# Kernel optimization log

Hardware: AMD Instinct MI355X
Metric: run time of the kernel (lower is better)

## Reference

```python
import jax, jax.numpy as jnp
from jax import lax
import numpy as np

B, T, D_IN, H, D_L1_IN = 128, 2048, 5, 128, 256


def _gru_layer(x, w_ih, w_hh, b_ih, b_hh, reverse):
    # x: [B,T,D]; w_ih: [3H,D]; w_hh: [3H,H]. PyTorch gate order: r, z, n.
    gx = jnp.einsum('btd,gd->btg', x, w_ih) + b_ih  # [B,T,3H] input projections, batched
    if reverse:
        gx = gx[:, ::-1]
    gx_t = jnp.swapaxes(gx, 0, 1)  # [T,B,3H]
    h0 = jnp.zeros((x.shape[0], H), x.dtype)

    def step(h, gxt):
        gh = h @ w_hh.T + b_hh  # [B,3H]
        r = jax.nn.sigmoid(gxt[:, :H] + gh[:, :H])
        z = jax.nn.sigmoid(gxt[:, H:2 * H] + gh[:, H:2 * H])
        n = jnp.tanh(gxt[:, 2 * H:] + r * gh[:, 2 * H:])
        h_new = (1.0 - z) * n + z * h
        return h_new, h_new

    _, ys = lax.scan(step, h0, gx_t)  # ys: [T,B,H]
    ys = jnp.swapaxes(ys, 0, 1)  # [B,T,H]
    if reverse:
        ys = ys[:, ::-1]
    return ys


def setup_inputs() -> dict:
    key = jax.random.key(0)
    ks = jax.random.split(key, 16)
    s0 = 1.0 / np.sqrt(H)

    def w(k, shape):
        return jax.random.uniform(k, shape, jnp.float32, -s0, s0)

    inp = {'seq': jax.random.normal(ks[0], (B, T, D_IN), jnp.float32)}
    # layer 0 forward / backward (input dim 5)
    inp['w_ih_l0f'] = w(ks[1], (3 * H, D_IN)); inp['w_hh_l0f'] = w(ks[2], (3 * H, H))
    inp['b_ih_l0f'] = w(ks[3], (3 * H,));      inp['b_hh_l0f'] = w(ks[4], (3 * H,))
    inp['w_ih_l0b'] = w(ks[5], (3 * H, D_IN)); inp['w_hh_l0b'] = w(ks[6], (3 * H, H))
    inp['b_ih_l0b'] = w(ks[7], (3 * H,));      inp['b_hh_l0b'] = w(ks[8], (3 * H,))
    # layer 1 forward / backward (input dim 256 = 2*H)
    inp['w_ih_l1f'] = w(ks[9], (3 * H, D_L1_IN));  inp['w_hh_l1f'] = w(ks[10], (3 * H, H))
    inp['b_ih_l1f'] = w(ks[11], (3 * H,));         inp['b_hh_l1f'] = w(ks[12], (3 * H,))
    inp['w_ih_l1b'] = w(ks[13], (3 * H, D_L1_IN)); inp['w_hh_l1b'] = w(ks[14], (3 * H, H))
    inp['b_ih_l1b'] = w(ks[15], (3 * H,));         inp['b_hh_l1b'] = w(ks[15], (3 * H,)) * 0.9
    # linear head
    kf = jax.random.split(ks[0], 2)
    inp['fc_w'] = w(kf[0], (1, 2 * H))
    inp['fc_b'] = w(kf[1], (1,))
    return inp


def reference(seq, w_ih_l0f, w_hh_l0f, b_ih_l0f, b_hh_l0f,
              w_ih_l0b, w_hh_l0b, b_ih_l0b, b_hh_l0b,
              w_ih_l1f, w_hh_l1f, b_ih_l1f, b_hh_l1f,
              w_ih_l1b, w_hh_l1b, b_ih_l1b, b_hh_l1b,
              fc_w, fc_b):
    # layer 0: bidirectional, concat directions
    y0f = _gru_layer(seq, w_ih_l0f, w_hh_l0f, b_ih_l0f, b_hh_l0f, reverse=False)
    y0b = _gru_layer(seq, w_ih_l0b, w_hh_l0b, b_ih_l0b, b_hh_l0b, reverse=True)
    y0 = jnp.concatenate([y0f, y0b], axis=-1)  # [B,T,256]
    # layer 1
    y1f = _gru_layer(y0, w_ih_l1f, w_hh_l1f, b_ih_l1f, b_hh_l1f, reverse=False)
    y1b = _gru_layer(y0, w_ih_l1b, w_hh_l1b, b_ih_l1b, b_hh_l1b, reverse=True)
    y1 = jnp.concatenate([y1f, y1b], axis=-1)  # [B,T,256]
    # head on last timestep
    return y1[:, -1, :] @ fc_w.T + fc_b  # [B,1]
```

## Files before the change

### kernel.cpp

```cpp
#include <hip/hip_runtime.h>
#include <hip/hip_fp16.h>
#include <cstdint>

#define B_   128
#define T_   2048
#define DIN  5
#define H_   128
#define G3   384
#define D1   256
#define CH   128
#define NCH  (T_ / CH)
#define LOG2CH 7

typedef _Float16 half8 __attribute__((ext_vector_type(8)));
typedef float f32x4 __attribute__((ext_vector_type(4)));

__device__ __forceinline__ float sigmoid_f(float x) {
    return __builtin_amdgcn_rcpf(1.0f + __expf(-x));
}
__device__ __forceinline__ float tanh_f(float x) {
    return 1.0f - 2.0f * __builtin_amdgcn_rcpf(__expf(2.0f * x) + 1.0f);
}
__device__ __forceinline__ unsigned long long pack4h(const float* h) {
    union { __half2 h2[2]; unsigned long long u; } pk;
    pk.h2[0] = __floats2half2_rn(h[0], h[1]);
    pk.h2[1] = __floats2half2_rn(h[2], h[3]);
    return pk.u;
}
__device__ __forceinline__ f32x4 h4_to_f(unsigned long long u) {
    union { unsigned long long u; __half2 h2[2]; } p; p.u = u;
    const float2 a = __half22float2(p.h2[0]);
    const float2 b = __half22float2(p.h2[1]);
    f32x4 r; r[0] = a.x; r[1] = a.y; r[2] = b.x; r[3] = b.y; return r;
}
__device__ __forceinline__ void fast_barrier() {
    asm volatile("s_waitcnt lgkmcnt(0)\n\ts_barrier" ::: "memory");
}

__global__ __launch_bounds__(512, 2) void scan0_mfma4(
    const float* __restrict__ seq,
    const float* __restrict__ wihf, const float* __restrict__ whhf,
    const float* __restrict__ bihf, const float* __restrict__ bhhf,
    const float* __restrict__ wihb, const float* __restrict__ whhb,
    const float* __restrict__ bihb, const float* __restrict__ bhhb,
    __half* __restrict__ y0)
{
    const int tid = threadIdx.x;
    const int w  = tid >> 6;
    const int l  = tid & 63;
    const int lo = l & 15;
    const int g  = l >> 4;
    const int dir = blockIdx.x >> 3;
    const int bg  = blockIdx.x & 7;

    const float* w_ih = dir ? wihb : wihf;
    const float* w_hh = dir ? whhb : whhf;
    const float* b_ih = dir ? bihb : bihf;
    const float* b_hh = dir ? bhhb : bhhf;

    __shared__ __align__(16) char smem[2 * 16 * 512];

    half8 a_r[5], a_z[5], a_n[5], a_x;
    {
        const int grow = w * 16 + lo;
#pragma unroll
        for (int c = 0; c < 5; ++c) {
            half8 vr, vz, vn;
#pragma unroll
            for (int j = 0; j < 8; ++j) {
                const int k = c * 32 + g * 8 + j;
                float fr, fz, fn;
                if (k < 128) {
                    fr = w_hh[grow * H_ + k];
                    fz = w_hh[(128 + grow) * H_ + k];
                    fn = w_hh[(256 + grow) * H_ + k];
                } else if (k < 133) {
                    fr = w_ih[grow * DIN + (k - 128)];
                    fz = w_ih[(128 + grow) * DIN + (k - 128)];
                    fn = 0.f;
                } else if (k == 133) {
                    fr = b_ih[grow] + b_hh[grow];
                    fz = b_ih[128 + grow] + b_hh[128 + grow];
                    fn = b_hh[256 + grow];
                } else { fr = 0.f; fz = 0.f; fn = 0.f; }
                vr[j] = (_Float16)fr; vz[j] = (_Float16)fz; vn[j] = (_Float16)fn;
            }
            a_r[c] = vr; a_z[c] = vz; a_n[c] = vn;
        }
        half8 vx;
#pragma unroll
        for (int j = 0; j < 8; ++j) {
            const int k = 128 + g * 8 + j;
            float f = 0.f;
            if (k < 133)       f = w_ih[(256 + grow) * DIN + (k - 128)];
            else if (k == 133) f = b_ih[256 + grow];
            vx[j] = (_Float16)f;
        }
        a_x = vx;
    }

#pragma unroll
    for (int q = 0; q < 2; ++q) {
        f32x4 z = {0.f, 0.f, 0.f, 0.f};
        *reinterpret_cast<f32x4*>(smem + tid * 32 + q * 16) = z;
    }
    __syncthreads();
    if (tid < 32) {
        const int row = tid & 15, bu = tid >> 4;
        *(_Float16*)(smem + bu * 8192 + row * 512 + (266 ^ ((row & 7) << 4))) =
            (_Float16)1.0f;
    }
    const bool stager = tid < 80;
    const int sb = tid / 5, sd = tid % 5;
    const size_t seqbase = (size_t)(bg * 16 + sb) * T_ * DIN + sd;
    float x_t1 = 0.f;
    if (stager) {
        const int tt0 = dir ? (T_ - 1) : 0;
        const float x0 = seq[seqbase + (size_t)tt0 * DIN];
        *(_Float16*)(smem + sb * 512 + ((256 + 2 * sd) ^ ((sb & 7) << 4))) =
            (_Float16)x0;
        const int tt1 = dir ? (T_ - 2) : 1;
        x_t1 = seq[seqbase + (size_t)tt1 * DIN];
    }
    __syncthreads();

    float h_old[4];
#pragma unroll
    for (int q = 0; q < 4; ++q) h_old[q] = 0.f;

    for (int t = 0; t < T_; ++t) {
        char* cur = smem + (t & 1) * 8192;
        char* nxt = smem + ((t + 1) & 1) * 8192;

        if (stager)
            *(_Float16*)(nxt + sb * 512 + ((256 + 2 * sd) ^ ((sb & 7) << 4))) =
                (_Float16)x_t1;

        half8 bf[5];
#pragma unroll
        for (int c = 0; c < 5; ++c)
            bf[c] = *reinterpret_cast<const half8*>(
                cur + lo * 512 + ((c * 64 + g * 16) ^ ((lo & 7) << 4)));

        float x_t2 = 0.f;
        if (stager) {
            const int t2 = (t + 2 < T_) ? t + 2 : T_ - 1;
            const int tt2 = dir ? (T_ - 1 - t2) : t2;
            x_t2 = seq[seqbase + (size_t)tt2 * DIN];
        }

        f32x4 zr = {0.f, 0.f, 0.f, 0.f};
        f32x4 accr = zr, accz = zr, accn = zr, accx;
#pragma unroll
        for (int c = 0; c < 5; ++c) {
            accr = __builtin_amdgcn_mfma_f32_16x16x32_f16(a_r[c], bf[c], accr, 0, 0, 0);
            accz = __builtin_amdgcn_mfma_f32_16x16x32_f16(a_z[c], bf[c], accz, 0, 0, 0);
            accn = __builtin_amdgcn_mfma_f32_16x16x32_f16(a_n[c], bf[c], accn, 0, 0, 0);
        }
        accx = __builtin_amdgcn_mfma_f32_16x16x32_f16(a_x, bf[4], zr, 0, 0, 0);

        const int tt = dir ? (T_ - 1 - t) : t;
        {
            float hn[4];
#pragma unroll
            for (int q = 0; q < 4; ++q) {
                const float r = sigmoid_f(accr[q]);
                const float z = sigmoid_f(accz[q]);
                const float n = tanh_f(accx[q] + r * accn[q]);
                hn[q] = n + z * (h_old[q] - n);
                h_old[q] = hn[q];
            }
            const int j0 = w * 16 + g * 4;
            const unsigned long long pu = pack4h(hn);
            *reinterpret_cast<unsigned long long*>(
                &y0[((size_t)(bg * 16 + lo) * T_ + tt) * D1 + dir * H_ + j0]) = pu;
            *reinterpret_cast<unsigned long long*>(
                nxt + lo * 512 + ((2 * j0) ^ ((lo & 7) << 4))) = pu;
        }
        x_t1 = x_t2;
        fast_barrier();
    }
}

__device__ __forceinline__ void scan1_role(
    char* smem,
    const __half* __restrict__ gxc,
    const float* __restrict__ whh, const float* __restrict__ bhh,
    float* __restrict__ h1, int c)
{
    __builtin_amdgcn_s_setprio(1);

    const int tid = threadIdx.x;
    const int w = tid >> 6, l = tid & 63;
    const int lo = l & 15, g = l >> 4;
    const int grp = blockIdx.x;

    half8 a_r[2][4], a_z[2][4], a_n[2][4];
    float br[2][4], bz[2][4], bn[2][4];
#pragma unroll
    for (int i = 0; i < 2; ++i) {
        const int grow = (2 * w + i) * 16 + lo;
#pragma unroll
        for (int cc = 0; cc < 4; ++cc) {
            half8 vr, vz, vn;
#pragma unroll
            for (int j = 0; j < 8; ++j) {
                const int k = cc * 32 + g * 8 + j;
                vr[j] = (_Float16)whh[grow * H_ + k];
                vz[j] = (_Float16)whh[(128 + grow) * H_ + k];
                vn[j] = (_Float16)whh[(256 + grow) * H_ + k];
            }
            a_r[i][cc] = vr; a_z[i][cc] = vz; a_n[i][cc] = vn;
        }
#pragma unroll
        for (int q = 0; q < 4; ++q) {
            const int gq = (2 * w + i) * 16 + g * 4 + q;
            br[i][q] = bhh[gq];
            bz[i][q] = bhh[128 + gq];
            bn[i][q] = bhh[256 + gq];
        }
    }

#pragma unroll
    for (int q = 0; q < 2; ++q) {
        f32x4 z = {0.f, 0.f, 0.f, 0.f};
        *reinterpret_cast<f32x4*>(smem + tid * 32 + q * 16) = z;
    }
    __syncthreads();

    float h_old[2][4];
    if (c == 0) {
#pragma unroll
        for (int i = 0; i < 2; ++i)
#pragma unroll
            for (int q = 0; q < 4; ++q) h_old[i][q] = 0.f;
    } else {
#pragma unroll
        for (int i = 0; i < 2; ++i) {
            const int j0 = (2 * w + i) * 16 + g * 4;
            const f32x4 hv = *reinterpret_cast<const f32x4*>(
                &h1[(grp * 16 + lo) * H_ + j0]);
            float hn[4];
#pragma unroll
            for (int q = 0; q < 4; ++q) { h_old[i][q] = hv[q]; hn[q] = hv[q]; }
            *reinterpret_cast<unsigned long long*>(
                smem + lo * 256 + ((2 * j0) ^ ((lo & 7) << 4))) = pack4h(hn);
        }
    }
    __syncthreads();

    const __half* gxl = gxc + (size_t)(grp * 16 + lo) * CH * G3;
    unsigned long long gxc_cur[6], gxc_nxt[6];
#pragma unroll
    for (int i = 0; i < 2; ++i) {
        const int gr0 = (2 * w + i) * 16 + g * 4;
        gxc_cur[i]     = *reinterpret_cast<const unsigned long long*>(gxl + gr0);
        gxc_cur[2 + i] = *reinterpret_cast<const unsigned long long*>(gxl + 128 + gr0);
        gxc_cur[4 + i] = *reinterpret_cast<const unsigned long long*>(gxl + 256 + gr0);
    }

    for (int t = 0; t < CH; ++t) {
        char* curb = smem + (t & 1) * 4096;
        char* nxtb = smem + ((t + 1) & 1) * 4096;

        half8 bf[4];
#pragma unroll
        for (int cc = 0; cc < 4; ++cc)
            bf[cc] = *reinterpret_cast<const half8*>(
                curb + lo * 256 + ((cc * 64 + g * 16) ^ ((lo & 7) << 4)));

        const int tn = (t + 1 < CH) ? t + 1 : t;
        const __half* p = gxl + (size_t)tn * G3;
#pragma unroll
        for (int i = 0; i < 2; ++i) {
            const int gr0 = (2 * w + i) * 16 + g * 4;
            gxc_nxt[i]     = *reinterpret_cast<const unsigned long long*>(p + gr0);
            gxc_nxt[2 + i] = *reinterpret_cast<const unsigned long long*>(p + 128 + gr0);
            gxc_nxt[4 + i] = *reinterpret_cast<const unsigned long long*>(p + 256 + gr0);
        }

        f32x4 accr[2], accz[2], accn[2];
#pragma unroll
        for (int i = 0; i < 2; ++i) {
            f32x4 zr = {0.f, 0.f, 0.f, 0.f};
            accr[i] = zr; accz[i] = zr; accn[i] = zr;
#pragma unroll
            for (int cc = 0; cc < 4; ++cc) {
                accr[i] = __builtin_amdgcn_mfma_f32_16x16x32_f16(a_r[i][cc], bf[cc], accr[i], 0, 0, 0);
                accz[i] = __builtin_amdgcn_mfma_f32_16x16x32_f16(a_z[i][cc], bf[cc], accz[i], 0, 0, 0);
                accn[i] = __builtin_amdgcn_mfma_f32_16x16x32_f16(a_n[i][cc], bf[cc], accn[i], 0, 0, 0);
            }
        }

#pragma unroll
        for (int i = 0; i < 2; ++i) {
            const f32x4 gr = h4_to_f(gxc_cur[i]);
            const f32x4 gz = h4_to_f(gxc_cur[2 + i]);
            const f32x4 gn = h4_to_f(gxc_cur[4 + i]);
            float hn[4];
#pragma unroll
            for (int q = 0; q < 4; ++q) {
                const float r = sigmoid_f(accr[i][q] + br[i][q] + gr[q]);
                const float z = sigmoid_f(accz[i][q] + bz[i][q] + gz[q]);
                const float n = tanh_f(gn[q] + r * (accn[i][q] + bn[i][q]));
                hn[q] = n + z * (h_old[i][q] - n);
                h_old[i][q] = hn[q];
            }
            const int j0 = (2 * w + i) * 16 + g * 4;
            *reinterpret_cast<unsigned long long*>(
                nxtb + lo * 256 + ((2 * j0) ^ ((lo & 7) << 4))) = pack4h(hn);
        }
#pragma unroll
        for (int i = 0; i < 6; ++i) gxc_cur[i] = gxc_nxt[i];
        fast_barrier();
    }

#pragma unroll
    for (int i = 0; i < 2; ++i) {
        const int j0 = (2 * w + i) * 16 + g * 4;
        f32x4 hv;
#pragma unroll
        for (int q = 0; q < 4; ++q) hv[q] = h_old[i][q];
        *reinterpret_cast<f32x4*>(&h1[(grp * 16 + lo) * H_ + j0]) = hv;
    }
    __builtin_amdgcn_s_setprio(0);
}

__device__ __forceinline__ void gemm_role(
    char* smem, int rb,
    const __half* __restrict__ A, const float* __restrict__ W,
    const float* __restrict__ bias, __half* __restrict__ C, int c0)
{
    _Float16 (*As)[32] = reinterpret_cast<_Float16(*)[32]>(smem);
    _Float16 (*Bs)[32] = reinterpret_cast<_Float16(*)[32]>(smem + 8192);
    const int tid = threadIdx.x;
    const int wave = tid >> 6, l = tid & 63;
    const int wm = wave >> 1, wn = wave & 1;
    const int lo = l & 15, g = l >> 4;
    const int m0 = (rb & 127) * 128, n0 = (rb >> 7) * 64;

    f32x4 acc[4][2];
#pragma unroll
    for (int mt = 0; mt < 4; ++mt)
#pragma unroll
        for (int nt = 0; nt < 2; ++nt) {
            f32x4 z = {0.f, 0.f, 0.f, 0.f};
            acc[mt][nt] = z;
        }

    for (int kc = 0; kc < 256; kc += 32) {
#pragma unroll
        for (int r2 = 0; r2 < 2; ++r2) {
            const int idx = tid + r2 * 256;
            const int row = idx >> 2, seg = idx & 3;
            const int m = m0 + row, bb = m >> LOG2CH, tlq = m & (CH - 1);
            const __half* src = A + ((size_t)bb * T_ + c0 + tlq) * D1 + kc + seg * 8;
            *reinterpret_cast<uint4*>(&As[row][seg * 8]) =
                *reinterpret_cast<const uint4*>(src);
        }
        {
            const int row = tid >> 2, seg = tid & 3;
            const float* srcw = W + (size_t)(n0 + row) * D1 + kc + seg * 8;
            const float4 u0 = *reinterpret_cast<const float4*>(srcw);
            const float4 u1 = *reinterpret_cast<const float4*>(srcw + 4);
            half8 hv;
            hv[0] = (_Float16)u0.x; hv[1] = (_Float16)u0.y;
            hv[2] = (_Float16)u0.z; hv[3] = (_Float16)u0.w;
            hv[4] = (_Float16)u1.x; hv[5] = (_Float16)u1.y;
            hv[6] = (_Float16)u1.z; hv[7] = (_Float16)u1.w;
            *reinterpret_cast<half8*>(&Bs[row][seg * 8]) = hv;
        }
        __syncthreads();
        half8 af[4], bfr[2];
#pragma unroll
        for (int mt = 0; mt < 4; ++mt)
            af[mt] = *reinterpret_cast<half8*>(&As[wm * 64 + mt * 16 + lo][g * 8]);
#pragma unroll
        for (int nt = 0; nt < 2; ++nt)
            bfr[nt] = *reinterpret_cast<half8*>(&Bs[wn * 32 + nt * 16 + lo][g * 8]);
#pragma unroll
        for (int mt = 0; mt < 4; ++mt)
#pragma unroll
            for (int nt = 0; nt < 2; ++nt)
                acc[mt][nt] = __builtin_amdgcn_mfma_f32_16x16x32_f16(
                    af[mt], bfr[nt], acc[mt][nt], 0, 0, 0);
        __syncthreads();
    }
#pragma unroll
    for (int nt = 0; nt < 2; ++nt) {
        const int n = n0 + wn * 32 + nt * 16 + lo;
        const float bv = bias[n];
#pragma unroll
        for (int mt = 0; mt < 4; ++mt) {
            const int mrow = m0 + wm * 64 + mt * 16 + g * 4;
#pragma unroll
            for (int q = 0; q < 4; ++q)
                C[(size_t)(mrow + q) * G3 + n] = __float2half(acc[mt][nt][q] + bv);
        }
    }
}

__global__ __launch_bounds__(256, 1) void fused_l1(
    const __half* __restrict__ y0,
    const float* __restrict__ W1f, const float* __restrict__ b1f,
    __half* __restrict__ gbufA, __half* __restrict__ gbufB,
    const float* __restrict__ whh, const float* __restrict__ bhh,
    float* __restrict__ h1, int ci_scan, int ci_gemm)
{
    __shared__ __align__(16) char smem[12288];
    if (blockIdx.x < 8) {
        if (ci_scan >= 0) {
            const __half* gxc = (ci_scan & 1) ? gbufB : gbufA;
            scan1_role(smem, gxc, whh, bhh, h1, ci_scan);
        }
    } else {
        if (ci_gemm < NCH) {
            __half* gxc = (ci_gemm & 1) ? gbufB : gbufA;
            gemm_role(smem, (int)blockIdx.x - 8, y0, W1f, b1f, gxc, ci_gemm * CH);
        }
    }
}

__global__ __launch_bounds__(384, 1) void back1_fc(
    const __half* __restrict__ y0, const float* __restrict__ h1,
    const float* __restrict__ w_ih_1b, const float* __restrict__ b_ih_1b,
    const float* __restrict__ b_hh_1b,
    const float* __restrict__ fc_w, const float* __restrict__ fc_b,
    float* __restrict__ out)
{
    const int g = threadIdx.x;
    const int b = blockIdx.x;
    __shared__ float ylast[D1];
    __shared__ float pre_rz[2 * H_];
    __shared__ float gxn[H_], ghn[H_];
    __shared__ float hb[H_];
    __shared__ float red[H_];

    if (g < D1) ylast[g] = __half2float(y0[((size_t)b * T_ + (T_ - 1)) * D1 + g]);
    __syncthreads();

    float accb = b_ih_1b[g];
    const float* wrow = w_ih_1b + (size_t)g * D1;
#pragma unroll 8
    for (int k = 0; k < D1; k += 4) {
        const float4 v = *reinterpret_cast<const float4*>(&ylast[k]);
        const float4 wv = *reinterpret_cast<const float4*>(&wrow[k]);
        accb += v.x * wv.x + v.y * wv.y + v.z * wv.z + v.w * wv.w;
    }
    const float bh2 = b_hh_1b[g];
    if (g < 2 * H_) pre_rz[g] = accb + bh2;
    else            { gxn[g - 2 * H_] = accb; ghn[g - 2 * H_] = bh2; }
    __syncthreads();
    if (g < H_) {
        const float r = sigmoid_f(pre_rz[g]);
        const float z = sigmoid_f(pre_rz[g + H_]);
        const float n = tanh_f(gxn[g] + r * ghn[g]);
        hb[g] = (1.0f - z) * n;
    }
    __syncthreads();
    if (g < H_) red[g] = h1[b * H_ + g] * fc_w[g] + hb[g] * fc_w[H_ + g];
    __syncthreads();
    if (g == 0) {
        float s = fc_b[0];
#pragma unroll 8
        for (int k = 0; k < H_; ++k) s += red[k];
        out[b] = s;
    }
}

extern "C" void kernel_launch(void* const* d_in, const int* in_sizes, int n_in,
                              void* d_out, int out_size, void* d_ws, size_t ws_size,
                              hipStream_t stream)
{
    const float* seq      = (const float*)d_in[0];
    const float* w_ih_l0f = (const float*)d_in[1];
    const float* w_hh_l0f = (const float*)d_in[2];
    const float* b_ih_l0f = (const float*)d_in[3];
    const float* b_hh_l0f = (const float*)d_in[4];
    const float* w_ih_l0b = (const float*)d_in[5];
    const float* w_hh_l0b = (const float*)d_in[6];
    const float* b_ih_l0b = (const float*)d_in[7];
    const float* b_hh_l0b = (const float*)d_in[8];
    const float* w_ih_l1f = (const float*)d_in[9];
    const float* w_hh_l1f = (const float*)d_in[10];
    const float* b_ih_l1f = (const float*)d_in[11];
    const float* b_hh_l1f = (const float*)d_in[12];
    const float* w_ih_l1b = (const float*)d_in[13];
    const float* b_ih_l1b = (const float*)d_in[15];
    const float* b_hh_l1b = (const float*)d_in[16];
    const float* fc_w     = (const float*)d_in[17];
    const float* fc_b     = (const float*)d_in[18];
    float* out = (float*)d_out;

    const size_t y0_bytes = (size_t)B_ * T_ * D1 * sizeof(__half);
    const size_t gx_bytes = (size_t)B_ * CH * G3 * sizeof(__half);
    __half* y0h   = (__half*)d_ws;
    __half* gbufA = (__half*)((char*)d_ws + y0_bytes);
    __half* gbufB = (__half*)((char*)d_ws + y0_bytes + gx_bytes);
    float*  h1    = (float*)((char*)d_ws + y0_bytes + 2 * gx_bytes);

    hipLaunchKernelGGL(scan0_mfma4, dim3(16), dim3(512), 0, stream,
        seq, w_ih_l0f, w_hh_l0f, b_ih_l0f, b_hh_l0f,
             w_ih_l0b, w_hh_l0b, b_ih_l0b, b_hh_l0b, y0h);

    for (int i = 0; i <= NCH; ++i) {
        hipLaunchKernelGGL(fused_l1, dim3(8 + 768), dim3(256), 0, stream,
            y0h, w_ih_l1f, b_ih_l1f, gbufA, gbufB,
            w_hh_l1f, b_hh_l1f, h1, i - 1, i);
    }

    hipLaunchKernelGGL(back1_fc, dim3(B_), dim3(384), 0, stream,
        y0h, h1, w_ih_l1b, b_ih_l1b, b_hh_l1b, fc_w, fc_b, out);
}
```

Baseline: 3.437 ms.

## Use larger layer-1 time chunks and persistent GEMM blocks to cut launches

Layer-1 time chunks are now 256 steps instead of 128 when the workspace is large enough, which halves the number of fused scan+GEMM launches and the grid barriers between them. The GEMM side no longer launches one block per tile. It uses a fixed 248 blocks that grid-stride over the tiles, so together with the 8 scan blocks the grid fits on the device at once. This trades launch and chunk-boundary overhead for a longer pipeline fill and drain, a larger intermediate buffer, and more GEMM work per block that must finish alongside the sequential scan.

```diff
diff --git a/kernel.cpp b/kernel.cpp
--- a/kernel.cpp
+++ b/kernel.cpp
@@ -8,9 +8,7 @@
 #define H_   128
 #define G3   384
 #define D1   256
-#define CH   128
-#define NCH  (T_ / CH)
-#define LOG2CH 7
+#define NGB  248
 
 typedef _Float16 half8 __attribute__((ext_vector_type(8)));
 typedef float f32x4 __attribute__((ext_vector_type(4)));
@@ -186,7 +184,7 @@
     char* smem,
     const __half* __restrict__ gxc,
     const float* __restrict__ whh, const float* __restrict__ bhh,
-    float* __restrict__ h1, int c)
+    float* __restrict__ h1, int c, int L)
 {
     __builtin_amdgcn_s_setprio(1);
 
@@ -249,7 +247,7 @@
     }
     __syncthreads();
 
-    const __half* gxl = gxc + (size_t)(grp * 16 + lo) * CH * G3;
+    const __half* gxl = gxc + (size_t)(grp * 16 + lo) * L * G3;
     unsigned long long gxc_cur[6], gxc_nxt[6];
 #pragma unroll
     for (int i = 0; i < 2; ++i) {
@@ -259,7 +257,7 @@
         gxc_cur[4 + i] = *reinterpret_cast<const unsigned long long*>(gxl + 256 + gr0);
     }
 
-    for (int t = 0; t < CH; ++t) {
+    for (int t = 0; t < L; ++t) {
         char* curb = smem + (t & 1) * 4096;
         char* nxtb = smem + ((t + 1) & 1) * 4096;
 
@@ -269,7 +267,7 @@
             bf[cc] = *reinterpret_cast<const half8*>(
                 curb + lo * 256 + ((cc * 64 + g * 16) ^ ((lo & 7) << 4)));
 
-        const int tn = (t + 1 < CH) ? t + 1 : t;
+        const int tn = (t + 1 < L) ? t + 1 : t;
         const __half* p = gxl + (size_t)tn * G3;
 #pragma unroll
         for (int i = 0; i < 2; ++i) {
@@ -329,7 +327,8 @@
 __device__ __forceinline__ void gemm_role(
     char* smem, int rb,
     const __half* __restrict__ A, const float* __restrict__ W,
-    const float* __restrict__ bias, __half* __restrict__ C, int c0)
+    const float* __restrict__ bias, __half* __restrict__ C,
+    int c0, int L, int log2L)
 {
     _Float16 (*As)[32] = reinterpret_cast<_Float16(*)[32]>(smem);
     _Float16 (*Bs)[32] = reinterpret_cast<_Float16(*)[32]>(smem + 8192);
@@ -337,7 +336,7 @@
     const int wave = tid >> 6, l = tid & 63;
     const int wm = wave >> 1, wn = wave & 1;
     const int lo = l & 15, g = l >> 4;
-    const int m0 = (rb & 127) * 128, n0 = (rb >> 7) * 64;
+    const int m0 = (rb & (L - 1)) * 128, n0 = (rb >> log2L) * 64;
 
     f32x4 acc[4][2];
 #pragma unroll
@@ -353,7 +352,7 @@
         for (int r2 = 0; r2 < 2; ++r2) {
             const int idx = tid + r2 * 256;
             const int row = idx >> 2, seg = idx & 3;
-            const int m = m0 + row, bb = m >> LOG2CH, tlq = m & (CH - 1);
+            const int m = m0 + row, bb = m >> log2L, tlq = m & (L - 1);
             const __half* src = A + ((size_t)bb * T_ + c0 + tlq) * D1 + kc + seg * 8;
             *reinterpret_cast<uint4*>(&As[row][seg * 8]) =
                 *reinterpret_cast<const uint4*>(src);
@@ -405,18 +404,21 @@
     const float* __restrict__ W1f, const float* __restrict__ b1f,
     __half* __restrict__ gbufA, __half* __restrict__ gbufB,
     const float* __restrict__ whh, const float* __restrict__ bhh,
-    float* __restrict__ h1, int ci_scan, int ci_gemm)
+    float* __restrict__ h1, int ci_scan, int ci_gemm,
+    int L, int log2L, int nch)
 {
     __shared__ __align__(16) char smem[12288];
     if (blockIdx.x < 8) {
         if (ci_scan >= 0) {
             const __half* gxc = (ci_scan & 1) ? gbufB : gbufA;
-            scan1_role(smem, gxc, whh, bhh, h1, ci_scan);
+            scan1_role(smem, gxc, whh, bhh, h1, ci_scan, L);
         }
     } else {
-        if (ci_gemm < NCH) {
+        if (ci_gemm < nch) {
             __half* gxc = (ci_gemm & 1) ? gbufB : gbufA;
-            gemm_role(smem, (int)blockIdx.x - 8, y0, W1f, b1f, gxc, ci_gemm * CH);
+            const int ntile = 6 * L;
+            for (int rb = (int)blockIdx.x - 8; rb < ntile; rb += NGB)
+                gemm_role(smem, rb, y0, W1f, b1f, gxc, ci_gemm * L, L, log2L);
         }
     }
 }
@@ -493,7 +495,16 @@
     float* out = (float*)d_out;
 
     const size_t y0_bytes = (size_t)B_ * T_ * D1 * sizeof(__half);
-    const size_t gx_bytes = (size_t)B_ * CH * G3 * sizeof(__half);
+    const size_t h1_bytes = (size_t)B_ * H_ * sizeof(float);
+
+    const size_t gx256 = (size_t)B_ * 256 * G3 * sizeof(__half);
+    const size_t gx128 = (size_t)B_ * 128 * G3 * sizeof(__half);
+    const bool big = ws_size >= y0_bytes + 2 * gx256 + h1_bytes;
+    const int L     = big ? 256 : 128;
+    const int log2L = big ? 8 : 7;
+    const int nch   = T_ / L;
+    const size_t gx_bytes = big ? gx256 : gx128;
+
     __half* y0h   = (__half*)d_ws;
     __half* gbufA = (__half*)((char*)d_ws + y0_bytes);
     __half* gbufB = (__half*)((char*)d_ws + y0_bytes + gx_bytes);
@@ -503,10 +514,10 @@
         seq, w_ih_l0f, w_hh_l0f, b_ih_l0f, b_hh_l0f,
              w_ih_l0b, w_hh_l0b, b_ih_l0b, b_hh_l0b, y0h);
 
-    for (int i = 0; i <= NCH; ++i) {
-        hipLaunchKernelGGL(fused_l1, dim3(8 + 768), dim3(256), 0, stream,
+    for (int i = 0; i <= nch; ++i) {
+        hipLaunchKernelGGL(fused_l1, dim3(8 + NGB), dim3(256), 0, stream,
             y0h, w_ih_l1f, b_ih_l1f, gbufA, gbufB,
-            w_hh_l1f, b_hh_l1f, h1, i - 1, i);
+            w_hh_l1f, b_hh_l1f, h1, i - 1, i, L, log2L, nch);
     }
 
     hipLaunchKernelGGL(back1_fc, dim3(B_), dim3(384), 0, stream,
```

Result: no change. 3.489 ms (+1.5%).
